# Performance work log

Hardware: AMD Instinct MI355X
Metric: run time of the kernel (lower is better)

Reference implementation:

```python
import jax, jax.numpy as jnp
import numpy as np

W, S, H, KH, D, BS, M, NB = 4, 32, 32, 8, 128, 16, 64, 2048  # ranks, seqs, heads, kv-heads, head_dim, block_size, blocks/seq, blocks/rank
SCALE = 1.0 / np.sqrt(D)


def setup_inputs() -> dict:
    key = jax.random.key(0)
    k1, k2, k3, k4, k5 = jax.random.split(key, 5)
    query = jax.random.normal(k1, (S, H, D), dtype=jnp.float32)
    key_cache = jax.random.normal(k2, (W, NB, KH, D, BS), dtype=jnp.float32)
    value_cache = jax.random.normal(k3, (W, NB, KH, D, BS), dtype=jnp.float32)
    block_tables = jax.random.randint(k4, (W, S, M), 0, NB, dtype=jnp.int32)
    context_lens = jnp.clip(jax.random.randint(k5, (W, S), 0, M * BS), 1, M * BS).astype(jnp.int32)
    return {"query": query, "key_cache": key_cache, "value_cache": value_cache,
            "block_tables": block_tables, "context_lens": context_lens}


def reference(query, key_cache, value_cache, block_tables, context_lens):
    num_seqs, num_heads, head_size = query.shape
    num_kv_heads = key_cache.shape[2]
    block_size = key_cache.shape[4]
    max_blocks = block_tables.shape[2]
    T = max_blocks * block_size  # max context per rank
    G = num_heads // num_kv_heads  # queries per kv head (GQA)
    q = query.reshape(num_seqs, num_kv_heads, G, head_size)
    t_idx = jnp.arange(T)

    def per_rank(kc, vc, bt, cl):
        # gather paged KV: [S, M, KH, D, BS] -> [S, KH, T, D]
        K = jnp.transpose(kc[bt], (0, 2, 1, 4, 3)).reshape(num_seqs, num_kv_heads, T, head_size)
        V = jnp.transpose(vc[bt], (0, 2, 1, 4, 3)).reshape(num_seqs, num_kv_heads, T, head_size)
        logits = jnp.einsum('skgd,sktd->skgt', q, K) * SCALE
        mask = t_idx[None, None, None, :] < cl[:, None, None, None]
        logits = jnp.where(mask, logits, -jnp.inf)
        m = jnp.max(logits, axis=-1)                      # per-rank max_logits
        p = jnp.exp(logits - m[..., None])
        se = jnp.sum(p, axis=-1)                          # per-rank exp_sums
        o = jnp.einsum('skgt,sktd->skgd', p, V) / se[..., None]  # per-rank normalized output
        return o, m, se

    o, m, se = jax.vmap(per_rank)(key_cache, value_cache, block_tables, context_lens)
    # distributed_paged_attention_v2_reduce: merge per-rank softmax states
    m_g = jnp.max(m, axis=0)
    w = se * jnp.exp(m - m_g[None])                       # [W, S, KH, G]
    out = jnp.einsum('wskgd,wskg->skgd', o, w) / jnp.sum(w, axis=0)[..., None]
    return out.reshape(num_seqs, num_heads, head_size)
```

## Files before the change

### kernel.cpp

```cpp
#include <hip/hip_runtime.h>
#include <math.h>

#define W_ 4
#define S_ 32
#define H_ 32
#define KH_ 8
#define D_ 128
#define BS_ 16
#define M_ 64
#define NB_ 2048
#define G_ (H_ / KH_)
#define NG_ (S_ * KH_ * G_)
#define SCALE_ 0.08838834764831845f

template <int NSB>
__global__ __launch_bounds__(256) void pa_phase1(
    const float* __restrict__ q, const float* __restrict__ kc,
    const float* __restrict__ vc, const int* __restrict__ bt,
    const int* __restrict__ cl, float* __restrict__ o_ws,
    float* __restrict__ se_ws) {
  const int wg = blockIdx.x;
  const int sb = wg % NSB;
  const int kh = (wg / NSB) % KH_;
  const int s = (wg / (NSB * KH_)) % S_;
  const int w = wg / (NSB * KH_ * S_);
  const int lane = threadIdx.x & 63;
  const int wv = threadIdx.x >> 6;
  const int d_sub = lane >> 2;
  const int tc = lane & 3;

  const int ctx = cl[w * S_ + s];
  const int nblk = (ctx + BS_ - 1) >> 4;
  const int pps = (nblk + NSB - 1) / NSB;
  const int j0 = sb * pps;
  const int j1 = min(j0 + pps, nblk);
  const int* bt_row = bt + (w * S_ + s) * M_;

  const float* qbase = q + ((size_t)s * H_ + kh * G_) * D_;
  float qreg[G_][8];
#pragma unroll
  for (int h = 0; h < G_; ++h)
#pragma unroll
    for (int i = 0; i < 8; ++i) qreg[h][i] = qbase[h * D_ + d_sub + 16 * i];

  float oacc[G_][8];
  float se[G_];
#pragma unroll
  for (int h = 0; h < G_; ++h) {
    se[h] = 0.f;
#pragma unroll
    for (int i = 0; i < 8; ++i) oacc[h][i] = 0.f;
  }

  for (int j = j0 + wv; j < j1; j += 4) {
    const int page = bt_row[j];
    const size_t pbase = ((((size_t)w * NB_ + page) * KH_) + kh) * (size_t)(D_ * BS_);
    const float* Kc = kc + pbase;
    const float* Vc = vc + pbase;

    float4 k4[8], v4[8];
#pragma unroll
    for (int i = 0; i < 8; ++i)
      k4[i] = *reinterpret_cast<const float4*>(Kc + (d_sub + 16 * i) * BS_ + 4 * tc);
#pragma unroll
    for (int i = 0; i < 8; ++i)
      v4[i] = *reinterpret_cast<const float4*>(Vc + (d_sub + 16 * i) * BS_ + 4 * tc);

    float4 a[G_];
#pragma unroll
    for (int h = 0; h < G_; ++h) a[h] = make_float4(0.f, 0.f, 0.f, 0.f);
#pragma unroll
    for (int i = 0; i < 8; ++i)
#pragma unroll
      for (int h = 0; h < G_; ++h) {
        a[h].x = fmaf(qreg[h][i], k4[i].x, a[h].x);
        a[h].y = fmaf(qreg[h][i], k4[i].y, a[h].y);
        a[h].z = fmaf(qreg[h][i], k4[i].z, a[h].z);
        a[h].w = fmaf(qreg[h][i], k4[i].w, a[h].w);
      }
#pragma unroll
    for (int off = 4; off <= 32; off <<= 1)
#pragma unroll
      for (int h = 0; h < G_; ++h) {
        a[h].x += __shfl_xor(a[h].x, off);
        a[h].y += __shfl_xor(a[h].y, off);
        a[h].z += __shfl_xor(a[h].z, off);
        a[h].w += __shfl_xor(a[h].w, off);
      }

    const int tbase = j * BS_ + 4 * tc;
    const bool in0 = tbase + 0 < ctx, in1 = tbase + 1 < ctx,
               in2 = tbase + 2 < ctx, in3 = tbase + 3 < ctx;

#pragma unroll
    for (int h = 0; h < G_; ++h) {
      const float p0 = in0 ? __expf(a[h].x * SCALE_) : 0.f;
      const float p1 = in1 ? __expf(a[h].y * SCALE_) : 0.f;
      const float p2 = in2 ? __expf(a[h].z * SCALE_) : 0.f;
      const float p3 = in3 ? __expf(a[h].w * SCALE_) : 0.f;
      se[h] += (p0 + p1) + (p2 + p3);
#pragma unroll
      for (int i = 0; i < 8; ++i) {
        oacc[h][i] = fmaf(p0, v4[i].x, oacc[h][i]);
        oacc[h][i] = fmaf(p1, v4[i].y, oacc[h][i]);
        oacc[h][i] = fmaf(p2, v4[i].z, oacc[h][i]);
        oacc[h][i] = fmaf(p3, v4[i].w, oacc[h][i]);
      }
    }
  }

#pragma unroll
  for (int off = 1; off <= 2; off <<= 1)
#pragma unroll
    for (int h = 0; h < G_; ++h) {
#pragma unroll
      for (int i = 0; i < 8; ++i) oacc[h][i] += __shfl_xor(oacc[h][i], off);
      se[h] += __shfl_xor(se[h], off);
    }

  const int r = (w * NSB + sb) * 4 + wv;
#pragma unroll
  for (int h = 0; h < G_; ++h) {
    const int grp = (s * KH_ + kh) * G_ + h;
    const size_t gidx = (size_t)r * NG_ + grp;
    if (tc == 0) {
#pragma unroll
      for (int i = 0; i < 8; ++i) o_ws[gidx * D_ + 16 * i + d_sub] = oacc[h][i];
    }
    if (lane == 0) se_ws[gidx] = se[h];
  }
}

template <int R>
__global__ __launch_bounds__(128) void pa_reduce(
    const float* __restrict__ o_ws, const float* __restrict__ se_ws,
    float* __restrict__ out) {
  const int grp = blockIdx.x;
  const int d = threadIdx.x;

  float denom = 0.f, acc = 0.f;
#pragma unroll 8
  for (int r = 0; r < R; ++r) {
    denom += se_ws[(size_t)r * NG_ + grp];
    acc += o_ws[((size_t)r * NG_ + grp) * D_ + d];
  }
  out[(size_t)grp * D_ + d] = acc / denom;
}

extern "C" void kernel_launch(void* const* d_in, const int* in_sizes, int n_in,
                              void* d_out, int out_size, void* d_ws, size_t ws_size,
                              hipStream_t stream) {
  (void)in_sizes; (void)n_in; (void)out_size;
  const float* q = (const float*)d_in[0];
  const float* kc = (const float*)d_in[1];
  const float* vc = (const float*)d_in[2];
  const int* bt = (const int*)d_in[3];
  const int* cl = (const int*)d_in[4];
  float* out = (float*)d_out;

  int nsb = 4;
  while (nsb > 1 &&
         (size_t)(W_ * nsb * 4) * NG_ * (D_ + 1) * sizeof(float) > ws_size)
    nsb >>= 1;

  const int R = W_ * nsb * 4;
  float* o_ws = (float*)d_ws;
  float* se_ws = o_ws + (size_t)R * NG_ * D_;

  const dim3 blk1(256), blk2(128), grid2(NG_);
  switch (nsb) {
    case 4:
      pa_phase1<4><<<dim3(W_ * S_ * KH_ * 4), blk1, 0, stream>>>(q, kc, vc, bt, cl, o_ws, se_ws);
      pa_reduce<64><<<grid2, blk2, 0, stream>>>(o_ws, se_ws, out);
      break;
    case 2:
      pa_phase1<2><<<dim3(W_ * S_ * KH_ * 2), blk1, 0, stream>>>(q, kc, vc, bt, cl, o_ws, se_ws);
      pa_reduce<32><<<grid2, blk2, 0, stream>>>(o_ws, se_ws, out);
      break;
    default:
      pa_phase1<1><<<dim3(W_ * S_ * KH_), blk1, 0, stream>>>(q, kc, vc, bt, cl, o_ws, se_ws);
      pa_reduce<16><<<grid2, blk2, 0, stream>>>(o_ws, se_ws, out);
      break;
  }
}
```

Before: 103.7 us.

## Reduce the four waves' partials in LDS and double-buffer KV page loads

Each workgroup's four waves now combine their partial output and exp-sum vectors in shared memory before writing. This cuts the phase-1 workspace writes and the reduce-kernel reads by a factor of four, and the reduce kernel's loop count shrinks to match. The KV page loop is restructured into a ping-pong register double buffer, so the next page's K/V loads are issued before the current page is computed. The extra float4 buffers raise register pressure and may reduce occupancy.

```diff
diff --git a/kernel.cpp b/kernel.cpp
--- a/kernel.cpp
+++ b/kernel.cpp
@@ -12,6 +12,57 @@
 #define G_ (H_ / KH_)
 #define NG_ (S_ * KH_ * G_)
 #define SCALE_ 0.08838834764831845f
+
+
+#define LOADPAGE(KB, VB, JJ)                                                  \
+  do {                                                                        \
+    const int page_ = bt_row[JJ];                                             \
+    const size_t pb_ =                                                        \
+        ((((size_t)w * NB_ + page_) * KH_) + kh) * (size_t)(D_ * BS_);        \
+    const float* Kc_ = kc + pb_;                                              \
+    const float* Vc_ = vc + pb_;                                              \
+    _Pragma("unroll") for (int i = 0; i < 8; ++i) KB[i] =                     \
+        *reinterpret_cast<const float4*>(Kc_ + (d_sub + 16 * i) * BS_ + 4 * tc); \
+    _Pragma("unroll") for (int i = 0; i < 8; ++i) VB[i] =                     \
+        *reinterpret_cast<const float4*>(Vc_ + (d_sub + 16 * i) * BS_ + 4 * tc); \
+  } while (0)
+
+#define COMPUTE(KB, VB, JJ)                                                   \
+  do {                                                                        \
+    float4 a_[G_];                                                            \
+    _Pragma("unroll") for (int h = 0; h < G_; ++h) a_[h] =                    \
+        make_float4(0.f, 0.f, 0.f, 0.f);                                      \
+    _Pragma("unroll") for (int i = 0; i < 8; ++i)                             \
+        _Pragma("unroll") for (int h = 0; h < G_; ++h) {                      \
+      a_[h].x = fmaf(qreg[h][i], KB[i].x, a_[h].x);                           \
+      a_[h].y = fmaf(qreg[h][i], KB[i].y, a_[h].y);                           \
+      a_[h].z = fmaf(qreg[h][i], KB[i].z, a_[h].z);                           \
+      a_[h].w = fmaf(qreg[h][i], KB[i].w, a_[h].w);                           \
+    }                                                                         \
+    _Pragma("unroll") for (int off = 4; off <= 32; off <<= 1)                 \
+        _Pragma("unroll") for (int h = 0; h < G_; ++h) {                      \
+      a_[h].x += __shfl_xor(a_[h].x, off);                                    \
+      a_[h].y += __shfl_xor(a_[h].y, off);                                    \
+      a_[h].z += __shfl_xor(a_[h].z, off);                                    \
+      a_[h].w += __shfl_xor(a_[h].w, off);                                    \
+    }                                                                         \
+    const int tbase_ = (JJ)*BS_ + 4 * tc;                                     \
+    const bool in0_ = tbase_ + 0 < ctx, in1_ = tbase_ + 1 < ctx,              \
+               in2_ = tbase_ + 2 < ctx, in3_ = tbase_ + 3 < ctx;              \
+    _Pragma("unroll") for (int h = 0; h < G_; ++h) {                          \
+      const float p0_ = in0_ ? __expf(a_[h].x * SCALE_) : 0.f;                \
+      const float p1_ = in1_ ? __expf(a_[h].y * SCALE_) : 0.f;                \
+      const float p2_ = in2_ ? __expf(a_[h].z * SCALE_) : 0.f;                \
+      const float p3_ = in3_ ? __expf(a_[h].w * SCALE_) : 0.f;                \
+      se[h] += (p0_ + p1_) + (p2_ + p3_);                                     \
+      _Pragma("unroll") for (int i = 0; i < 8; ++i) {                         \
+        oacc[h][i] = fmaf(p0_, VB[i].x, oacc[h][i]);                          \
+        oacc[h][i] = fmaf(p1_, VB[i].y, oacc[h][i]);                          \
+        oacc[h][i] = fmaf(p2_, VB[i].z, oacc[h][i]);                          \
+        oacc[h][i] = fmaf(p3_, VB[i].w, oacc[h][i]);                          \
+      }                                                                       \
+    }                                                                         \
+  } while (0)
 
 template <int NSB>
 __global__ __launch_bounds__(256) void pa_phase1(
@@ -29,6 +80,9 @@
   const int d_sub = lane >> 2;
   const int tc = lane & 3;
 
+  __shared__ float lds_o[4][G_][D_];
+  __shared__ float lds_se[4][G_];
+
   const int ctx = cl[w * S_ + s];
   const int nblk = (ctx + BS_ - 1) >> 4;
   const int pps = (nblk + NSB - 1) / NSB;
@@ -52,61 +106,19 @@
     for (int i = 0; i < 8; ++i) oacc[h][i] = 0.f;
   }
 
-  for (int j = j0 + wv; j < j1; j += 4) {
-    const int page = bt_row[j];
-    const size_t pbase = ((((size_t)w * NB_ + page) * KH_) + kh) * (size_t)(D_ * BS_);
-    const float* Kc = kc + pbase;
-    const float* Vc = vc + pbase;
-
-    float4 k4[8], v4[8];
-#pragma unroll
-    for (int i = 0; i < 8; ++i)
-      k4[i] = *reinterpret_cast<const float4*>(Kc + (d_sub + 16 * i) * BS_ + 4 * tc);
-#pragma unroll
-    for (int i = 0; i < 8; ++i)
-      v4[i] = *reinterpret_cast<const float4*>(Vc + (d_sub + 16 * i) * BS_ + 4 * tc);
-
-    float4 a[G_];
-#pragma unroll
-    for (int h = 0; h < G_; ++h) a[h] = make_float4(0.f, 0.f, 0.f, 0.f);
-#pragma unroll
-    for (int i = 0; i < 8; ++i)
-#pragma unroll
-      for (int h = 0; h < G_; ++h) {
-        a[h].x = fmaf(qreg[h][i], k4[i].x, a[h].x);
-        a[h].y = fmaf(qreg[h][i], k4[i].y, a[h].y);
-        a[h].z = fmaf(qreg[h][i], k4[i].z, a[h].z);
-        a[h].w = fmaf(qreg[h][i], k4[i].w, a[h].w);
-      }
-#pragma unroll
-    for (int off = 4; off <= 32; off <<= 1)
-#pragma unroll
-      for (int h = 0; h < G_; ++h) {
-        a[h].x += __shfl_xor(a[h].x, off);
-        a[h].y += __shfl_xor(a[h].y, off);
-        a[h].z += __shfl_xor(a[h].z, off);
-        a[h].w += __shfl_xor(a[h].w, off);
-      }
-
-    const int tbase = j * BS_ + 4 * tc;
-    const bool in0 = tbase + 0 < ctx, in1 = tbase + 1 < ctx,
-               in2 = tbase + 2 < ctx, in3 = tbase + 3 < ctx;
-
-#pragma unroll
-    for (int h = 0; h < G_; ++h) {
-      const float p0 = in0 ? __expf(a[h].x * SCALE_) : 0.f;
-      const float p1 = in1 ? __expf(a[h].y * SCALE_) : 0.f;
-      const float p2 = in2 ? __expf(a[h].z * SCALE_) : 0.f;
-      const float p3 = in3 ? __expf(a[h].w * SCALE_) : 0.f;
-      se[h] += (p0 + p1) + (p2 + p3);
-#pragma unroll
-      for (int i = 0; i < 8; ++i) {
-        oacc[h][i] = fmaf(p0, v4[i].x, oacc[h][i]);
-        oacc[h][i] = fmaf(p1, v4[i].y, oacc[h][i]);
-        oacc[h][i] = fmaf(p2, v4[i].z, oacc[h][i]);
-        oacc[h][i] = fmaf(p3, v4[i].w, oacc[h][i]);
-      }
-    }
+  float4 kA[8], vA[8], kB[8], vB[8];
+  int j = j0 + wv;
+  if (j < j1) LOADPAGE(kA, vA, j);
+  while (j < j1) {
+    int jn = j + 4;
+    if (jn < j1) LOADPAGE(kB, vB, jn);
+    COMPUTE(kA, vA, j);
+    j = jn;
+    if (j >= j1) break;
+    jn = j + 4;
+    if (jn < j1) LOADPAGE(kA, vA, jn);
+    COMPUTE(kB, vB, j);
+    j = jn;
   }
 
 #pragma unroll
@@ -118,16 +130,31 @@
       se[h] += __shfl_xor(se[h], off);
     }
 
-  const int r = (w * NSB + sb) * 4 + wv;
-#pragma unroll
-  for (int h = 0; h < G_; ++h) {
+  if (tc == 0) {
+#pragma unroll
+    for (int h = 0; h < G_; ++h) {
+#pragma unroll
+      for (int i = 0; i < 8; ++i) lds_o[wv][h][16 * i + d_sub] = oacc[h][i];
+      if (d_sub == 0) lds_se[wv][h] = se[h];
+    }
+  }
+  __syncthreads();
+
+  const int r = w * NSB + sb;
+#pragma unroll
+  for (int e = 0; e < 2; ++e) {
+    const int idx = threadIdx.x + 256 * e;
+    const int h = idx >> 7, d = idx & 127;
+    const float v =
+        (lds_o[0][h][d] + lds_o[1][h][d]) + (lds_o[2][h][d] + lds_o[3][h][d]);
     const int grp = (s * KH_ + kh) * G_ + h;
-    const size_t gidx = (size_t)r * NG_ + grp;
-    if (tc == 0) {
-#pragma unroll
-      for (int i = 0; i < 8; ++i) o_ws[gidx * D_ + 16 * i + d_sub] = oacc[h][i];
-    }
-    if (lane == 0) se_ws[gidx] = se[h];
+    o_ws[((size_t)r * NG_ + grp) * D_ + d] = v;
+  }
+  if (threadIdx.x < G_) {
+    const int h = threadIdx.x;
+    const int grp = (s * KH_ + kh) * G_ + h;
+    se_ws[(size_t)r * NG_ + grp] =
+        (lds_se[0][h] + lds_se[1][h]) + (lds_se[2][h] + lds_se[3][h]);
   }
 }
 
@@ -139,7 +166,7 @@
   const int d = threadIdx.x;
 
   float denom = 0.f, acc = 0.f;
-#pragma unroll 8
+#pragma unroll
   for (int r = 0; r < R; ++r) {
     denom += se_ws[(size_t)r * NG_ + grp];
     acc += o_ws[((size_t)r * NG_ + grp) * D_ + d];
@@ -160,10 +187,10 @@
 
   int nsb = 4;
   while (nsb > 1 &&
-         (size_t)(W_ * nsb * 4) * NG_ * (D_ + 1) * sizeof(float) > ws_size)
+         (size_t)(W_ * nsb) * NG_ * (D_ + 1) * sizeof(float) > ws_size)
     nsb >>= 1;
 
-  const int R = W_ * nsb * 4;
+  const int R = W_ * nsb;
   float* o_ws = (float*)d_ws;
   float* se_ws = o_ws + (size_t)R * NG_ * D_;
 
@@ -171,15 +198,15 @@
   switch (nsb) {
     case 4:
       pa_phase1<4><<<dim3(W_ * S_ * KH_ * 4), blk1, 0, stream>>>(q, kc, vc, bt, cl, o_ws, se_ws);
-      pa_reduce<64><<<grid2, blk2, 0, stream>>>(o_ws, se_ws, out);
+      pa_reduce<16><<<grid2, blk2, 0, stream>>>(o_ws, se_ws, out);
       break;
     case 2:
       pa_phase1<2><<<dim3(W_ * S_ * KH_ * 2), blk1, 0, stream>>>(q, kc, vc, bt, cl, o_ws, se_ws);
-      pa_reduce<32><<<grid2, blk2, 0, stream>>>(o_ws, se_ws, out);
+      pa_reduce<8><<<grid2, blk2, 0, stream>>>(o_ws, se_ws, out);
       break;
     default:
       pa_phase1<1><<<dim3(W_ * S_ * KH_), blk1, 0, stream>>>(q, kc, vc, bt, cl, o_ws, se_ws);
-      pa_reduce<16><<<grid2, blk2, 0, stream>>>(o_ws, se_ws, out);
+      pa_reduce<4><<<grid2, blk2, 0, stream>>>(o_ws, se_ws, out);
       break;
   }
 }
```

Result: slower. 141.7 us (+36.6%).
